# Kernel optimization log

Hardware: AMD Instinct MI355X
Metric: run time of the kernel (lower is better)

The kernel has to match this reference:

```python
import jax, jax.numpy as jnp
import numpy as np

B, I, H = 8192, 1024, 1024

def setup_inputs() -> dict:
    key = jax.random.key(0)
    ks = jax.random.split(key, 6)
    s_in = 1.0 / np.sqrt(I)
    s_h = 1.0 / np.sqrt(H)
    return {
        "x": jax.random.normal(ks[0], (B, I), jnp.float32),
        "h_prev": jax.random.normal(ks[1], (B, H), jnp.float32),
        "c_prev": jax.random.normal(ks[2], (B, H), jnp.float32),
        "Wx": jax.random.normal(ks[3], (4, H, I), jnp.float32) * s_in,   # gate order: input, forget, cell, output
        "Wh": jax.random.normal(ks[4], (4, H, H), jnp.float32) * s_h,
        "bh": jax.random.normal(ks[5], (4, H), jnp.float32) * s_h,
    }

def reference(x, h_prev, c_prev, Wx, Wh, bh):
    # Fused: 2 batched GEMMs for all 4 gates -> [B, 4, H]
    gates = (jnp.einsum('bi,ghi->bgh', x, Wx)
             + jnp.einsum('bk,ghk->bgh', h_prev, Wh)
             + bh[None, :, :])
    i = jax.nn.sigmoid(gates[:, 0])
    f = jax.nn.sigmoid(gates[:, 1])
    g = jnp.tanh(gates[:, 2])
    o = jax.nn.sigmoid(gates[:, 3])
    c_next = f * c_prev + i * g
    h_next = o * jnp.tanh(c_next)
    return (h_next, c_next)
```

## Files before the change

### kernel.cpp

```cpp
#include <hip/hip_runtime.h>
#include <hip/hip_bf16.h>
#include <stdint.h>

#define B_DIM 8192
#define I_DIM 1024
#define H_DIM 1024
#define KTOT  2048
#define NTILES 32

typedef __attribute__((ext_vector_type(8))) short short8;
typedef __attribute__((ext_vector_type(4))) float f32x4;

static __device__ __forceinline__ short f2b(float f) {
    __bf16 h = (__bf16)f;
    return __builtin_bit_cast(short, h);
}

static __device__ __forceinline__ short8 pack8(float4 a, float4 b) {
    short8 s;
    s[0] = f2b(a.x); s[1] = f2b(a.y); s[2] = f2b(a.z); s[3] = f2b(a.w);
    s[4] = f2b(b.x); s[5] = f2b(b.y); s[6] = f2b(b.z); s[7] = f2b(b.w);
    return s;
}

static __device__ __forceinline__ float sigmoid_f(float x) {
    return 1.0f / (1.0f + __expf(-x));
}

static __device__ __forceinline__ float tanh_fast(float x) {
    x = fminf(fmaxf(x, -15.0f), 15.0f);
    float e = __expf(2.0f * x);
    return (e - 1.0f) / (e + 1.0f);
}

static __device__ __forceinline__ void load_lds16(const void* gptr, void* lptr) {
    __builtin_amdgcn_global_load_lds(
        (const __attribute__((address_space(1))) uint32_t*)gptr,
        (__attribute__((address_space(3))) uint32_t*)lptr, 16, 0, 0);
}

__global__ __launch_bounds__(256) void convert_kernel(
    const float* __restrict__ x, const float* __restrict__ h,
    const float* __restrict__ wx, const float* __restrict__ wh,
    short* __restrict__ Aw, short* __restrict__ Bw)
{
    const int64_t nx = (int64_t)B_DIM * I_DIM / 8;
    const int64_t nw = (int64_t)4 * H_DIM * I_DIM / 8;
    const int64_t total = 2 * nx + 2 * nw;
    for (int64_t g = (int64_t)blockIdx.x * blockDim.x + threadIdx.x; g < total;
         g += (int64_t)gridDim.x * blockDim.x) {
        const float* src;
        short* dst;
        if (g < nx) {
            int64_t r = g >> 7, kc = (g & 127) * 8;
            src = x + g * 8; dst = Aw + r * 2048 + kc;
        } else if (g < 2 * nx) {
            int64_t gg = g - nx;
            int64_t r = gg >> 7, kc = (gg & 127) * 8;
            src = h + gg * 8; dst = Aw + r * 2048 + 1024 + kc;
        } else if (g < 2 * nx + nw) {
            int64_t gg = g - 2 * nx;
            int64_t r = gg >> 7, kc = (gg & 127) * 8;
            src = wx + gg * 8; dst = Bw + r * 2048 + kc;
        } else {
            int64_t gg = g - 2 * nx - nw;
            int64_t r = gg >> 7, kc = (gg & 127) * 8;
            src = wh + gg * 8; dst = Bw + r * 2048 + 1024 + kc;
        }
        float4 v0 = ((const float4*)src)[0];
        float4 v1 = ((const float4*)src)[1];
        *(short8*)dst = pack8(v0, v1);
    }
}


#define AOFF(d, kp, f) ((d) * 16384 + (kp) * 8192 + (f) * 512)
#define BOFF(d, kp, f) (32768 + (d) * 16384 + (kp) * 8192 + (f) * 512)

#define STAGE_A(dn, kh, tkp) \
    load_lds16(aSrc0 + (size_t)(tkp) * 64 + (kh) * 32, &smem[AOFF(dn, kh, 2 * w)]); \
    load_lds16(aSrc1 + (size_t)(tkp) * 64 + (kh) * 32, &smem[AOFF(dn, kh, 2 * w + 1)]);

#define STAGE_B(dn, kh, tkp) \
    load_lds16(bSrc0 + (size_t)(tkp) * 64 + (kh) * 32, &smem[BOFF(dn, kh, 2 * w)]); \
    load_lds16(bSrc1 + (size_t)(tkp) * 64 + (kh) * 32, &smem[BOFF(dn, kh, 2 * w + 1)]);

#define VM4 asm volatile("s_waitcnt vmcnt(4)" ::: "memory");

#define PHASE(d, kp, mh, STAGE_STMT, EXTRAWAIT) do { \
    short8 av[4], bv[4]; \
    _Pragma("unroll") \
    for (int i = 0; i < 4; ++i) \
        av[i] = *(const short8*)&smem[AOFF(d, kp, wm * 8 + (mh) * 4 + i) + lane * 8]; \
    _Pragma("unroll") \
    for (int j = 0; j < 4; ++j) \
        bv[j] = *(const short8*)&smem[BOFF(d, kp, wn * 4 + j) + lane * 8]; \
    STAGE_STMT \
    __builtin_amdgcn_s_barrier(); \
    asm volatile("s_waitcnt lgkmcnt(0)" ::: "memory"); \
    __builtin_amdgcn_sched_barrier(0); \
    __builtin_amdgcn_s_setprio(1); \
    _Pragma("unroll") \
    for (int i = 0; i < 4; ++i) \
        _Pragma("unroll") \
        for (int j = 0; j < 4; ++j) \
            acc[(mh) * 4 + i][j] = __builtin_amdgcn_mfma_f32_16x16x32_bf16( \
                av[i], bv[j], acc[(mh) * 4 + i][j], 0, 0, 0); \
    __builtin_amdgcn_s_setprio(0); \
    EXTRAWAIT \
    __builtin_amdgcn_s_barrier(); \
} while (0)

__global__ __launch_bounds__(512, 2) void lstm_gemm8_kernel(
    const short* __restrict__ Aw, const short* __restrict__ Bw,
    const float* __restrict__ cprev, const float* __restrict__ bh,
    float* __restrict__ out)
{
    extern __shared__ __align__(16) short smem[];

    int bid = blockIdx.x;
    bid = (bid & 7) * 64 + (bid >> 3);
    const int bm = bid >> 4;
    const int bn = bid & 15;
    const int m0 = bm * 256;
    const int h0 = bn * 64;

    const int t    = threadIdx.x;
    const int lane = t & 63;
    const int w    = t >> 6;
    const int wm   = w >> 2;
    const int wn   = w & 3;
    const int lc   = lane & 15;
    const int lk   = lane >> 4;

    const short* aSrc0 = Aw + (size_t)(m0 + (2 * w + 0) * 16 + lc) * 2048 + lk * 8;
    const short* aSrc1 = Aw + (size_t)(m0 + (2 * w + 1) * 16 + lc) * 2048 + lk * 8;
    const int cf0 = 2 * w, cf1 = 2 * w + 1;
    const short* bSrc0 = Bw + (size_t)((cf0 & 3) * 1024 + h0 + ((cf0 >> 2) << 4) + lc) * 2048 + lk * 8;
    const short* bSrc1 = Bw + (size_t)((cf1 & 3) * 1024 + h0 + ((cf1 >> 2) << 4) + lc) * 2048 + lk * 8;

    f32x4 acc[8][4] = {};

    STAGE_A(0, 0, 0)
    STAGE_B(0, 0, 0)
    STAGE_A(0, 1, 0)
    STAGE_B(0, 1, 0)
    asm volatile("s_waitcnt vmcnt(4)" ::: "memory");
    __builtin_amdgcn_s_barrier();

    #pragma unroll 1
    for (int tk2 = 0; tk2 < 16; ++tk2) {
        const int t1  = 2 * tk2 + 1;
        const int tp1 = (t1 + 1 < NTILES) ? t1 + 1 : t1;
        PHASE(0, 0, 0, STAGE_A(1, 0, t1), );
        PHASE(0, 0, 1, STAGE_B(1, 0, t1), VM4);
        PHASE(0, 1, 0, STAGE_A(1, 1, t1), );
        PHASE(0, 1, 1, STAGE_B(1, 1, t1), VM4);
        PHASE(1, 0, 0, STAGE_A(0, 0, tp1), );
        PHASE(1, 0, 1, STAGE_B(0, 0, tp1), VM4);
        PHASE(1, 1, 0, STAGE_A(0, 1, tp1), );
        PHASE(1, 1, 1, STAGE_B(0, 1, tp1), VM4);
    }
    asm volatile("s_waitcnt vmcnt(0)" ::: "memory");

    const int rg = lane >> 4;
    const int h  = h0 + wn * 16 + lc;
    const float b_i = bh[0 * H_DIM + h];
    const float b_f = bh[1 * H_DIM + h];
    const float b_g = bh[2 * H_DIM + h];
    const float b_o = bh[3 * H_DIM + h];

    #pragma unroll
    for (int mf = 0; mf < 8; ++mf) {
        #pragma unroll
        for (int r = 0; r < 4; ++r) {
            const int row = m0 + wm * 128 + mf * 16 + rg * 4 + r;
            const float pi = acc[mf][0][r] + b_i;
            const float pf = acc[mf][1][r] + b_f;
            const float pg = acc[mf][2][r] + b_g;
            const float po = acc[mf][3][r] + b_o;
            const float iv = sigmoid_f(pi);
            const float fv = sigmoid_f(pf);
            const float gv = tanh_fast(pg);
            const float ov = sigmoid_f(po);
            const float cp = cprev[(size_t)row * H_DIM + h];
            const float cn = fv * cp + iv * gv;
            const float hn = ov * tanh_fast(cn);
            out[(size_t)row * H_DIM + h] = hn;
            out[(size_t)B_DIM * H_DIM + (size_t)row * H_DIM + h] = cn;
        }
    }
}

static __device__ __forceinline__ int swz(int row, int k) {
    int byte = (row << 7) + (k << 1);
    byte ^= (row & 7) << 4;
    return byte >> 1;
}

__global__ __launch_bounds__(256, 2) void lstm_fallback_kernel(
    const float* __restrict__ x, const float* __restrict__ hprev,
    const float* __restrict__ cprev, const float* __restrict__ Wx,
    const float* __restrict__ Wh, const float* __restrict__ bh,
    float* __restrict__ out)
{
    __shared__ __align__(16) short As[128 * 64];
    __shared__ __align__(16) short Bs[128 * 64];

    int bid = blockIdx.x;
    bid = (bid & 7) * 256 + (bid >> 3);
    const int mt = bid >> 5;
    const int ht = bid & 31;
    const int m0 = mt * 128;
    const int h0 = ht * 32;

    const int t    = threadIdx.x;
    const int lane = t & 63;
    const int w    = t >> 6;
    const int wr   = w >> 1;
    const int wc   = w & 1;

    const int srow = t >> 3;
    const int sk   = (t & 7) * 8;

    f32x4 acc[4][4] = {};

    #pragma unroll 1
    for (int phase = 0; phase < 2; ++phase) {
        const float* __restrict__ Ap = phase ? hprev : x;
        const float* __restrict__ Bp = phase ? Wh : Wx;
        #pragma unroll 1
        for (int kk = 0; kk < 1024; kk += 64) {
            __syncthreads();
            #pragma unroll
            for (int p = 0; p < 4; ++p) {
                const int row = srow + p * 32;
                const float4* src = (const float4*)(Ap + (size_t)(m0 + row) * I_DIM + kk + sk);
                *(short8*)&As[swz(row, sk)] = pack8(src[0], src[1]);
            }
            #pragma unroll
            for (int p = 0; p < 4; ++p) {
                const int n    = srow + p * 32;
                const int gate = (n >> 4) & 3;
                const int hcol = h0 + ((n >> 6) << 4) + (n & 15);
                const float4* src = (const float4*)(Bp + (size_t)((gate << 10) + hcol) * 1024 + kk + sk);
                *(short8*)&Bs[swz(n, sk)] = pack8(src[0], src[1]);
            }
            __syncthreads();
            #pragma unroll
            for (int ks = 0; ks < 2; ++ks) {
                const int kb = ks * 32 + ((lane >> 4) << 3);
                short8 a[4], b[4];
                #pragma unroll
                for (int m = 0; m < 4; ++m)
                    a[m] = *(const short8*)&As[swz(wr * 64 + m * 16 + (lane & 15), kb)];
                #pragma unroll
                for (int j = 0; j < 4; ++j)
                    b[j] = *(const short8*)&Bs[swz(wc * 64 + j * 16 + (lane & 15), kb)];
                #pragma unroll
                for (int m = 0; m < 4; ++m)
                    #pragma unroll
                    for (int j = 0; j < 4; ++j)
                        acc[m][j] = __builtin_amdgcn_mfma_f32_16x16x32_bf16(a[m], b[j], acc[m][j], 0, 0, 0);
            }
        }
    }

    const int cl = lane & 15;
    const int rg = lane >> 4;
    const int h  = h0 + wc * 16 + cl;
    const float b_i = bh[0 * H_DIM + h];
    const float b_f = bh[1 * H_DIM + h];
    const float b_g = bh[2 * H_DIM + h];
    const float b_o = bh[3 * H_DIM + h];

    #pragma unroll
    for (int m = 0; m < 4; ++m) {
        #pragma unroll
        for (int r = 0; r < 4; ++r) {
            const int row = m0 + wr * 64 + m * 16 + rg * 4 + r;
            const float pi = acc[m][0][r] + b_i;
            const float pf = acc[m][1][r] + b_f;
            const float pg = acc[m][2][r] + b_g;
            const float po = acc[m][3][r] + b_o;
            const float iv = sigmoid_f(pi);
            const float fv = sigmoid_f(pf);
            const float gv = tanh_fast(pg);
            const float ov = sigmoid_f(po);
            const float cp = cprev[(size_t)row * H_DIM + h];
            const float cn = fv * cp + iv * gv;
            const float hn = ov * tanh_fast(cn);
            out[(size_t)row * H_DIM + h] = hn;
            out[(size_t)B_DIM * H_DIM + (size_t)row * H_DIM + h] = cn;
        }
    }
}

extern "C" void kernel_launch(void* const* d_in, const int* in_sizes, int n_in,
                              void* d_out, int out_size, void* d_ws, size_t ws_size,
                              hipStream_t stream) {
    const float* x     = (const float*)d_in[0];
    const float* hprev = (const float*)d_in[1];
    const float* cprev = (const float*)d_in[2];
    const float* Wx    = (const float*)d_in[3];
    const float* Wh    = (const float*)d_in[4];
    const float* bh    = (const float*)d_in[5];
    float* out = (float*)d_out;

    const size_t need = ((size_t)B_DIM * 2048 + (size_t)4096 * 2048) * sizeof(short);
    if (ws_size >= need && d_ws != nullptr) {
        (void)hipFuncSetAttribute((const void*)lstm_gemm8_kernel,
                                  hipFuncAttributeMaxDynamicSharedMemorySize, 131072);
        short* Aw = (short*)d_ws;
        short* Bw = Aw + (size_t)B_DIM * 2048;
        hipLaunchKernelGGL(convert_kernel, dim3(2048), dim3(256), 0, stream,
                           x, hprev, Wx, Wh, Aw, Bw);
        hipLaunchKernelGGL(lstm_gemm8_kernel, dim3(512), dim3(512), 131072, stream,
                           Aw, Bw, cprev, bh, out);
    } else {
        hipLaunchKernelGGL(lstm_fallback_kernel, dim3(2048), dim3(256), 0, stream,
                           x, hprev, cprev, Wx, Wh, bh, out);
    }
}
```

Before: 173.8 us.

## Replace eight-phase barrier pipeline with per-tile double-buffered stage-compute loop

Swaps the fine-grained eight-phase schedule for a simpler double-buffered one. The old schedule interleaved half-tile global-to-LDS loads with MFMA groups, separated by two barriers and partial vmcnt waits each phase. The new one issues the whole next tile's loads up front, computes both k-halves of the current tile, then waits vmcnt(0) and takes one barrier per tile. This cuts barrier and waitcnt overhead and gives the compiler a larger MFMA block to schedule. In exchange it drops the setprio hints and the finer overlap, and each tile ends with a full drain of outstanding loads.

```diff
diff --git a/kernel.cpp b/kernel.cpp
--- a/kernel.cpp
+++ b/kernel.cpp
@@ -85,29 +85,39 @@
     load_lds16(bSrc0 + (size_t)(tkp) * 64 + (kh) * 32, &smem[BOFF(dn, kh, 2 * w)]); \
     load_lds16(bSrc1 + (size_t)(tkp) * 64 + (kh) * 32, &smem[BOFF(dn, kh, 2 * w + 1)]);
 
-#define VM4 asm volatile("s_waitcnt vmcnt(4)" ::: "memory");
-
-#define PHASE(d, kp, mh, STAGE_STMT, EXTRAWAIT) do { \
-    short8 av[4], bv[4]; \
+#define TILE(d, tn) do { \
+    STAGE_A(d ^ 1, 0, tn) \
+    STAGE_B(d ^ 1, 0, tn) \
+    STAGE_A(d ^ 1, 1, tn) \
+    STAGE_B(d ^ 1, 1, tn) \
     _Pragma("unroll") \
-    for (int i = 0; i < 4; ++i) \
-        av[i] = *(const short8*)&smem[AOFF(d, kp, wm * 8 + (mh) * 4 + i) + lane * 8]; \
-    _Pragma("unroll") \
-    for (int j = 0; j < 4; ++j) \
-        bv[j] = *(const short8*)&smem[BOFF(d, kp, wn * 4 + j) + lane * 8]; \
-    STAGE_STMT \
-    __builtin_amdgcn_s_barrier(); \
-    asm volatile("s_waitcnt lgkmcnt(0)" ::: "memory"); \
-    __builtin_amdgcn_sched_barrier(0); \
-    __builtin_amdgcn_s_setprio(1); \
-    _Pragma("unroll") \
-    for (int i = 0; i < 4; ++i) \
+    for (int kp = 0; kp < 2; ++kp) { \
+        short8 bv[4]; \
         _Pragma("unroll") \
         for (int j = 0; j < 4; ++j) \
-            acc[(mh) * 4 + i][j] = __builtin_amdgcn_mfma_f32_16x16x32_bf16( \
-                av[i], bv[j], acc[(mh) * 4 + i][j], 0, 0, 0); \
-    __builtin_amdgcn_s_setprio(0); \
-    EXTRAWAIT \
+            bv[j] = *(const short8*)&smem[BOFF(d, kp, wn * 4 + j) + lane * 8]; \
+        short8 av[4]; \
+        _Pragma("unroll") \
+        for (int i = 0; i < 4; ++i) \
+            av[i] = *(const short8*)&smem[AOFF(d, kp, wm * 8 + i) + lane * 8]; \
+        _Pragma("unroll") \
+        for (int i = 0; i < 4; ++i) \
+            _Pragma("unroll") \
+            for (int j = 0; j < 4; ++j) \
+                acc[i][j] = __builtin_amdgcn_mfma_f32_16x16x32_bf16( \
+                    av[i], bv[j], acc[i][j], 0, 0, 0); \
+        short8 aw[4]; \
+        _Pragma("unroll") \
+        for (int i = 0; i < 4; ++i) \
+            aw[i] = *(const short8*)&smem[AOFF(d, kp, wm * 8 + 4 + i) + lane * 8]; \
+        _Pragma("unroll") \
+        for (int i = 0; i < 4; ++i) \
+            _Pragma("unroll") \
+            for (int j = 0; j < 4; ++j) \
+                acc[4 + i][j] = __builtin_amdgcn_mfma_f32_16x16x32_bf16( \
+                    aw[i], bv[j], acc[4 + i][j], 0, 0, 0); \
+    } \
+    asm volatile("s_waitcnt vmcnt(0)" ::: "memory"); \
     __builtin_amdgcn_s_barrier(); \
 } while (0)
 
@@ -145,23 +155,16 @@
     STAGE_B(0, 0, 0)
     STAGE_A(0, 1, 0)
     STAGE_B(0, 1, 0)
-    asm volatile("s_waitcnt vmcnt(4)" ::: "memory");
+    asm volatile("s_waitcnt vmcnt(0)" ::: "memory");
     __builtin_amdgcn_s_barrier();
 
     #pragma unroll 1
     for (int tk2 = 0; tk2 < 16; ++tk2) {
         const int t1  = 2 * tk2 + 1;
         const int tp1 = (t1 + 1 < NTILES) ? t1 + 1 : t1;
-        PHASE(0, 0, 0, STAGE_A(1, 0, t1), );
-        PHASE(0, 0, 1, STAGE_B(1, 0, t1), VM4);
-        PHASE(0, 1, 0, STAGE_A(1, 1, t1), );
-        PHASE(0, 1, 1, STAGE_B(1, 1, t1), VM4);
-        PHASE(1, 0, 0, STAGE_A(0, 0, tp1), );
-        PHASE(1, 0, 1, STAGE_B(0, 0, tp1), VM4);
-        PHASE(1, 1, 0, STAGE_A(0, 1, tp1), );
-        PHASE(1, 1, 1, STAGE_B(0, 1, tp1), VM4);
-    }
-    asm volatile("s_waitcnt vmcnt(0)" ::: "memory");
+        TILE(0, t1);
+        TILE(1, tp1);
+    }
 
     const int rg = lane >> 4;
     const int h  = h0 + wn * 16 + lc;
```

Result: slower. 192.7 us (+10.9%).
